# Kernel optimization log

Hardware: AMD Instinct MI355X
Metric: run time of the kernel (lower is better)

## Reference

```python
import jax, jax.numpy as jnp
import numpy as np

# --- model dims (from init_kwargs: d_model=2048, num_heads=16, d_conv=4, expand_v=2) ---
D_MODEL = 2048
N_HEADS = 16
D_HEAD = D_MODEL // N_HEADS          # 128
EXPAND_V = 2
KEY_DIM = N_HEADS * D_HEAD           # 2048
VALUE_DIM = KEY_DIM * EXPAND_V       # 4096
HEAD_V = D_HEAD * EXPAND_V           # 256
D_CONV = 4
CONV_CH = 2 * KEY_DIM + VALUE_DIM    # 8192 (q,k,v channels)
TOTAL_PROJ = 2 * KEY_DIM + 2 * VALUE_DIM + 2 * N_HEADS  # 12320
SPLITS = np.cumsum([KEY_DIM, KEY_DIM, VALUE_DIM, VALUE_DIM, N_HEADS]).tolist()


def setup_inputs() -> dict:
    key = jax.random.key(0)
    k0, k1, k2, k3 = jax.random.split(key, 4)
    B, L = 2, 2048
    return {
        "hidden_states": jax.random.normal(k0, (B, L, D_MODEL), jnp.float32),
        "W_qkvgba": jax.random.normal(k1, (D_MODEL, TOTAL_PROJ), jnp.float32) * 0.02,
        "W_conv": jax.random.normal(k2, (CONV_CH, D_CONV), jnp.float32) * 0.1,
        "A_log": jax.random.normal(k3, (N_HEADS,), jnp.float32) * 0.1,
        "dt_bias": jnp.zeros((N_HEADS,), jnp.float32),
    }


def _l2norm(x, eps=1e-6):
    return x * jax.lax.rsqrt(jnp.sum(x * x, axis=-1, keepdims=True) + eps)


def reference(hidden_states, W_qkvgba, W_conv, A_log, dt_bias):
    B, L, _ = hidden_states.shape
    # fused qkv / gate / beta / A projection
    proj = hidden_states @ W_qkvgba                      # [B, L, 12320]
    q, k, v, gate, b, A = jnp.split(proj, SPLITS, axis=-1)

    # depthwise causal short conv over q,k,v channels, then SiLU
    qkv = jnp.concatenate([q, k, v], axis=-1)            # [B, L, CONV_CH]
    x = qkv.transpose(0, 2, 1)                           # [B, C, L]
    kern = W_conv[:, None, :]                            # [C, 1, D_CONV]
    y = jax.lax.conv_general_dilated(
        x, kern, window_strides=(1,), padding=[(D_CONV - 1, 0)],
        feature_group_count=CONV_CH)
    y = jax.nn.silu(y).transpose(0, 2, 1)                # [B, L, C]
    q, k, v = jnp.split(y, [KEY_DIM, 2 * KEY_DIM], axis=-1)

    q = q.reshape(B, L, N_HEADS, D_HEAD)
    k = k.reshape(B, L, N_HEADS, D_HEAD)
    v = v.reshape(B, L, N_HEADS, HEAD_V)

    # L2 norm of q,k (use_qk_l2norm_in_kernel=True)
    q = _l2norm(q)
    k = _l2norm(k)
    scale = D_HEAD ** -0.5

    beta = jax.nn.sigmoid(b)                             # [B, L, H]
    g = -jnp.exp(A_log) * jax.nn.softplus(A + dt_bias)   # [B, L, H] (log decay <= 0)

    # gated delta-rule recurrence over time (scan); state S: [B, H, dk, dv]
    qT = q.transpose(1, 0, 2, 3)
    kT = k.transpose(1, 0, 2, 3)
    vT = v.transpose(1, 0, 2, 3)
    gT = g.transpose(1, 0, 2)
    bT = beta.transpose(1, 0, 2)

    def step(S, inp):
        qt, kt, vt, gt, bt = inp
        S = S * jnp.exp(gt)[..., None, None]
        kv = jnp.einsum('bhk,bhkv->bhv', kt, S)          # current memory readout at k
        delta = (vt - kv) * bt[..., None]                # delta-rule error, gated by beta
        S = S + jnp.einsum('bhk,bhv->bhkv', kt, delta)
        ot = jnp.einsum('bhk,bhkv->bhv', qt * scale, S)
        return S, ot

    S0 = jnp.zeros((B, N_HEADS, D_HEAD, HEAD_V), jnp.float32)
    _, oT = jax.lax.scan(step, S0, (qT, kT, vT, gT, bT))
    o = oT.transpose(1, 0, 2, 3)                         # [B, L, H, HEAD_V]

    # output gating: o * silu(gate)
    gate = gate.reshape(B, L, N_HEADS, HEAD_V)
    return o * jax.nn.silu(gate)
```

## Files before the change

### kernel.cpp

```cpp
#include <hip/hip_runtime.h>
#include <hip/hip_bf16.h>
#include <hip/hip_fp16.h>
#include <math.h>

#define L_SEQ 2048
#define DM    2048
#define NH    16
#define DH    128
#define HVD   256
#define NPROJ 12320
#define QKVW  8192
#define GW    4128

#define NTILE_N 97
#define KSTEPS  64

typedef _Float16 v8h __attribute__((ext_vector_type(8)));
typedef float f32x4 __attribute__((ext_vector_type(4)));

__device__ __forceinline__ void gload_lds16(const void* g, void* l) {
  __builtin_amdgcn_global_load_lds((const __attribute__((address_space(1))) void*)g,
                                   (__attribute__((address_space(3))) void*)l, 16, 0, 0);
}

__device__ __forceinline__ void splitw(float x, unsigned short& h, unsigned short& l) {
  _Float16 hh = (_Float16)x;
  _Float16 ll = (_Float16)(x - (float)hh);
  h = *(unsigned short*)&hh;
  l = *(unsigned short*)&ll;
}
__device__ __forceinline__ float h2f(unsigned short u) {
  return (float)(*(_Float16*)&u);
}

#define MFMA3(acc, ah, al, bh_, bl_)                                          \
  acc = __builtin_amdgcn_mfma_f32_16x16x32_f16(ah, bh_, acc, 0, 0, 0);        \
  acc = __builtin_amdgcn_mfma_f32_16x16x32_f16(ah, bl_, acc, 0, 0, 0);        \
  acc = __builtin_amdgcn_mfma_f32_16x16x32_f16(al, bh_, acc, 0, 0, 0);

__global__ __launch_bounds__(256) void pack_A_k(const float* __restrict__ H, _Float16* __restrict__ Ap) {
  const int mtile = blockIdx.x >> 6, kstep = blockIdx.x & 63;
  const size_t base = (size_t)blockIdx.x * 2 * 4096;
#pragma unroll
  for (int it = 0; it < 2; ++it) {
    int s = threadIdx.x + it * 256;
    int g = s >> 7, r = s & 127;
    const float* src = H + ((size_t)(mtile * 128 + r)) * 2048 + kstep * 32 + g * 8;
    float4 x0 = *(const float4*)src;
    float4 x1 = *(const float4*)(src + 4);
    float xs[8] = {x0.x, x0.y, x0.z, x0.w, x1.x, x1.y, x1.z, x1.w};
    v8h hi, lo;
#pragma unroll
    for (int j = 0; j < 8; ++j) {
      float v = xs[j] * 16.f;
      _Float16 h = (_Float16)v;
      hi[j] = h;
      lo[j] = (_Float16)(v - (float)h);
    }
    *(v8h*)(Ap + base + g * 1024 + r * 8) = hi;
    *(v8h*)(Ap + base + 4096 + g * 1024 + r * 8) = lo;
  }
}

__global__ __launch_bounds__(256) void pack_B_k(const float* __restrict__ W, _Float16* __restrict__ Bp) {
  const int ntile = blockIdx.x >> 6, kstep = blockIdx.x & 63;
  const size_t base = (size_t)blockIdx.x * 2 * 4096;
#pragma unroll
  for (int it = 0; it < 2; ++it) {
    int s = threadIdx.x + it * 256;
    int g = s >> 7, col = s & 127;
    int n = ntile * 128 + col;
    v8h hi, lo;
#pragma unroll
    for (int j = 0; j < 8; ++j) {
      int k = kstep * 32 + g * 8 + j;
      float v = (n < NPROJ) ? W[(size_t)k * NPROJ + n] * 1024.f : 0.f;
      _Float16 h = (_Float16)v;
      hi[j] = h;
      lo[j] = (_Float16)(v - (float)h);
    }
    *(v8h*)(Bp + base + g * 1024 + col * 8) = hi;
    *(v8h*)(Bp + base + 4096 + g * 1024 + col * 8) = lo;
  }
}

__global__ __launch_bounds__(512, 2) void gemm256_k(const _Float16* __restrict__ Ap,
                                                    const _Float16* __restrict__ Bp,
                                                    float* __restrict__ Cq,
                                                    float* __restrict__ Cg) {
  __shared__ _Float16 lds[2][32768];
  const int tid = threadIdx.x;
  const int supM = blockIdx.x & 15;
  const int supN = blockIdx.x >> 4;
  const int w = tid >> 6, lane = tid & 63;
  const int wm = w >> 2, wn = w & 3;
  const int lr = lane & 15, g16 = lane >> 4;

  f32x4 acc[8][4];
#pragma unroll
  for (int i = 0; i < 8; ++i)
#pragma unroll
    for (int j = 0; j < 4; ++j) acc[i][j] = (f32x4){0.f, 0.f, 0.f, 0.f};

  const size_t Ab0 = (size_t)(2 * supM) * KSTEPS * 8192;
  const size_t Ab1 = Ab0 + (size_t)KSTEPS * 8192;
  const size_t Bb0 = (size_t)(2 * supN) * KSTEPS * 8192;
  const size_t Bb1 = Bb0 + (size_t)KSTEPS * 8192;
  const int so = tid * 8;

#define STG(KS, BUF)                                                           \
  {                                                                            \
    const size_t ko = (size_t)(KS) * 8192;                                     \
    gload_lds16(Ap + Ab0 + ko + so,        &lds[BUF][so]);                     \
    gload_lds16(Ap + Ab0 + ko + so + 4096, &lds[BUF][so + 4096]);              \
    gload_lds16(Ap + Ab1 + ko + so,        &lds[BUF][8192 + so]);              \
    gload_lds16(Ap + Ab1 + ko + so + 4096, &lds[BUF][8192 + so + 4096]);       \
    gload_lds16(Bp + Bb0 + ko + so,        &lds[BUF][16384 + so]);             \
    gload_lds16(Bp + Bb0 + ko + so + 4096, &lds[BUF][16384 + so + 4096]);      \
    gload_lds16(Bp + Bb1 + ko + so,        &lds[BUF][24576 + so]);             \
    gload_lds16(Bp + Bb1 + ko + so + 4096, &lds[BUF][24576 + so + 4096]);      \
  }

  STG(0, 0);
  asm volatile("s_waitcnt vmcnt(0)" ::: "memory");
  __builtin_amdgcn_sched_barrier(0);
  __builtin_amdgcn_s_barrier();
  __builtin_amdgcn_sched_barrier(0);

  const int aoffB = wm * 8192 + lr * 8 + g16 * 1024;
  const int boffB = 16384 + (wn >> 1) * 8192 + ((wn & 1) * 64 + lr) * 8 + g16 * 1024;

  for (int kstep = 0; kstep < KSTEPS; ++kstep) {
    const int p = kstep & 1;
    if (kstep + 1 < KSTEPS) STG(kstep + 1, p ^ 1);

    v8h ah[8], al[8];
#pragma unroll
    for (int mb = 0; mb < 8; ++mb) {
      ah[mb] = *(const v8h*)&lds[p][aoffB + mb * 128];
      al[mb] = *(const v8h*)&lds[p][aoffB + mb * 128 + 4096];
    }
#pragma unroll
    for (int nt = 0; nt < 4; ++nt) {
      v8h bh = *(const v8h*)&lds[p][boffB + nt * 128];
      v8h bl = *(const v8h*)&lds[p][boffB + nt * 128 + 4096];
#pragma unroll
      for (int mb = 0; mb < 8; ++mb) {
        MFMA3(acc[mb][nt], ah[mb], al[mb], bh, bl);
      }
    }
    asm volatile("s_waitcnt vmcnt(0)" ::: "memory");
    __builtin_amdgcn_sched_barrier(0);
    __builtin_amdgcn_s_barrier();
    __builtin_amdgcn_sched_barrier(0);
  }
#undef STG

  const float sc = 1.f / 16384.f;
#pragma unroll
  for (int mb = 0; mb < 8; ++mb) {
#pragma unroll
    for (int nt = 0; nt < 4; ++nt) {
      int col = supN * 256 + wn * 64 + nt * 16 + lr;
#pragma unroll
      for (int r = 0; r < 4; ++r) {
        int row = supM * 256 + wm * 128 + mb * 16 + g16 * 4 + r;
        float v = acc[mb][nt][r] * sc;
        if (col < QKVW) Cq[(size_t)row * QKVW + col] = v;
        else            Cg[(size_t)row * GW + (col - QKVW)] = v;
      }
    }
  }
}

__global__ __launch_bounds__(256) void tail_k(const _Float16* __restrict__ Ap,
                                              const _Float16* __restrict__ Bp,
                                              float* __restrict__ partial) {
  __shared__ _Float16 lds[16384];
  const int bid = blockIdx.x;
  const int kseg = bid >> 5, mtile = bid & 31;
  const int tid = threadIdx.x;
  const int wid = tid >> 6, lane = tid & 63, lr = lane & 15, g16 = lane >> 4;

  f32x4 acc[2][2];
#pragma unroll
  for (int i = 0; i < 2; ++i)
#pragma unroll
    for (int j = 0; j < 2; ++j) acc[i][j] = (f32x4){0.f, 0.f, 0.f, 0.f};

  const _Float16* Asrc = Ap + ((size_t)(mtile * KSTEPS) * 2) * 4096 + tid * 8;
  const _Float16* Bsrc = Bp + ((size_t)(96 * KSTEPS) * 2) * 4096 + tid * 8;

  for (int ks = kseg * 16; ks < kseg * 16 + 16; ++ks) {
    __syncthreads();
#pragma unroll
    for (int r = 0; r < 4; ++r) {
      gload_lds16(Asrc + (size_t)ks * 8192 + r * 2048, &lds[r * 2048 + tid * 8]);
      gload_lds16(Bsrc + (size_t)ks * 8192 + r * 2048, &lds[8192 + r * 2048 + tid * 8]);
    }
    __syncthreads();
    const int abase = g16 * 1024;
#pragma unroll
    for (int fm = 0; fm < 2; ++fm) {
      int row = wid * 32 + fm * 16 + lr;
      v8h ah = *(const v8h*)&lds[abase + row * 8];
      v8h al = *(const v8h*)&lds[4096 + abase + row * 8];
#pragma unroll
      for (int fn = 0; fn < 2; ++fn) {
        int col = fn * 16 + lr;
        v8h bh = *(const v8h*)&lds[8192 + abase + col * 8];
        v8h bl = *(const v8h*)&lds[12288 + abase + col * 8];
        MFMA3(acc[fm][fn], ah, al, bh, bl);
      }
    }
  }

  const float sc = 1.f / 16384.f;
#pragma unroll
  for (int fm = 0; fm < 2; ++fm)
#pragma unroll
    for (int fn = 0; fn < 2; ++fn) {
      int col = fn * 16 + lr;
#pragma unroll
      for (int r = 0; r < 4; ++r) {
        int row = mtile * 128 + wid * 32 + fm * 16 + g16 * 4 + r;
        partial[((size_t)kseg * 4096 + row) * 32 + col] = acc[fm][fn][r] * sc;
      }
    }
}

__global__ __launch_bounds__(64) void conv_qk_k(
    const float* __restrict__ projQKV, const float* __restrict__ Wc,
    _Float16* __restrict__ qh, _Float16* __restrict__ ql,
    _Float16* __restrict__ kh, _Float16* __restrict__ kl)
{
  const int b = blockIdx.z, hg = blockIdx.y, tc = blockIdx.x;
  const int lane = threadIdx.x;
  const int ch = hg * 128 + lane * 2;
  float4 Wa = *(const float4*)(Wc + (size_t)ch * 4);
  float4 Wb = *(const float4*)(Wc + (size_t)ch * 4 + 4);
  const int t0 = tc * 64;
  const float* P = projQKV + (size_t)b * L_SEQ * QKVW + ch;
  float2 w0 = make_float2(0.f, 0.f), w1 = w0, w2 = w0;
  if (t0 >= 3) w0 = *(const float2*)(P + (size_t)(t0 - 3) * QKVW);
  if (t0 >= 2) w1 = *(const float2*)(P + (size_t)(t0 - 2) * QKVW);
  if (t0 >= 1) w2 = *(const float2*)(P + (size_t)(t0 - 1) * QKVW);
  const bool isq = hg < 16;
  const int h = isq ? hg : hg - 16;
  _Float16* dh = (isq ? qh : kh) + (((size_t)b * NH + h) * L_SEQ) * 128;
  _Float16* dl = (isq ? ql : kl) + (((size_t)b * NH + h) * L_SEQ) * 128;
  const float sc = (isq ? 0.08838834764831845f : 1.f) * 1024.f;
  for (int t = t0; t < t0 + 64; ++t) {
    float2 x = *(const float2*)(P + (size_t)t * QKVW);
    float y0 = w0.x * Wa.x + w1.x * Wa.y + w2.x * Wa.z + x.x * Wa.w;
    float y1 = w0.y * Wb.x + w1.y * Wb.y + w2.y * Wb.z + x.y * Wb.w;
    w0 = w1; w1 = w2; w2 = x;
    y0 = y0 / (1.f + expf(-y0));
    y1 = y1 / (1.f + expf(-y1));
    float ss = y0 * y0 + y1 * y1;
#pragma unroll
    for (int off = 1; off < 64; off <<= 1) ss += __shfl_xor(ss, off);
    float nrm = sc / sqrtf(ss + 1e-6f);
    unsigned short h0, l0, h1, l1;
    splitw(y0 * nrm, h0, l0);
    splitw(y1 * nrm, h1, l1);
    int idx = t * 128 + ((lane * 2) ^ ((t & 7) << 3));
    *(unsigned int*)&dh[idx] = (unsigned int)h0 | ((unsigned int)h1 << 16);
    *(unsigned int*)&dl[idx] = (unsigned int)l0 | ((unsigned int)l1 << 16);
  }
}

__global__ __launch_bounds__(256) void conv_v_k(
    const float* __restrict__ projQKV, const float* __restrict__ Wc,
    float* __restrict__ vn)
{
  const int b = blockIdx.z, cg = blockIdx.y, tc = blockIdx.x;
  const int vc = (cg * 256 + threadIdx.x) * 4;
  const int ch = 4096 + vc;
  float4 Wv0 = *(const float4*)(Wc + (size_t)ch * 4);
  float4 Wv1 = *(const float4*)(Wc + (size_t)ch * 4 + 4);
  float4 Wv2 = *(const float4*)(Wc + (size_t)ch * 4 + 8);
  float4 Wv3 = *(const float4*)(Wc + (size_t)ch * 4 + 12);
  const int t0 = tc * 64;
  const float* P = projQKV + (size_t)b * L_SEQ * QKVW + ch;
  float4 w0 = make_float4(0.f, 0.f, 0.f, 0.f), w1 = w0, w2 = w0;
  if (t0 >= 3) w0 = *(const float4*)(P + (size_t)(t0 - 3) * QKVW);
  if (t0 >= 2) w1 = *(const float4*)(P + (size_t)(t0 - 2) * QKVW);
  if (t0 >= 1) w2 = *(const float4*)(P + (size_t)(t0 - 1) * QKVW);
  const int h = vc >> 8, vcol = vc & 255;
  float* dst = vn + (((size_t)b * NH + h) * L_SEQ) * HVD + vcol;
  for (int t = t0; t < t0 + 64; ++t) {
    float4 x = *(const float4*)(P + (size_t)t * QKVW);
    float4 y;
    y.x = w0.x * Wv0.x + w1.x * Wv0.y + w2.x * Wv0.z + x.x * Wv0.w;
    y.y = w0.y * Wv1.x + w1.y * Wv1.y + w2.y * Wv1.z + x.y * Wv1.w;
    y.z = w0.z * Wv2.x + w1.z * Wv2.y + w2.z * Wv2.z + x.z * Wv2.w;
    y.w = w0.w * Wv3.x + w1.w * Wv3.y + w2.w * Wv3.z + x.w * Wv3.w;
    w0 = w1; w1 = w2; w2 = x;
    y.x = y.x / (1.f + expf(-y.x));
    y.y = y.y / (1.f + expf(-y.y));
    y.z = y.z / (1.f + expf(-y.z));
    y.w = y.w / (1.f + expf(-y.w));
    *(float4*)(dst + (size_t)t * HVD) = y;
  }
}

__global__ __launch_bounds__(256) void beta_g_k(
    const float* __restrict__ partial, const float* __restrict__ A_log,
    const float* __restrict__ dt_bias, float* __restrict__ beta, float* __restrict__ g_out)
{
  int idx = blockIdx.x * 256 + threadIdx.x;
  if (idx >= 2 * NH * L_SEQ) return;
  int t = idx & (L_SEQ - 1);
  int h = (idx >> 11) & (NH - 1);
  int b = idx >> 15;
  size_t row = (size_t)(b * L_SEQ + t);
  float bv = 0.f, av = 0.f;
#pragma unroll
  for (int s = 0; s < 4; ++s) {
    bv += partial[((size_t)s * 4096 + row) * 32 + h];
    av += partial[((size_t)s * 4096 + row) * 32 + 16 + h];
  }
  float be = 1.f / (1.f + expf(-bv));
  float xx = av + dt_bias[h];
  float sp = (xx > 20.f) ? xx : log1pf(expf(xx));
  float g = -expf(A_log[h]) * sp;
  beta[idx] = be;
  g_out[idx] = g;
}

__global__ __launch_bounds__(256) void p1_k(
    const _Float16* __restrict__ kh_g, const _Float16* __restrict__ kl_g,
    const _Float16* __restrict__ qh_g, const _Float16* __restrict__ ql_g,
    const float* __restrict__ g_arr, const float* __restrict__ beta_arr,
    _Float16* __restrict__ Tg_h, _Float16* __restrict__ Tg_l,
    _Float16* __restrict__ Hg_h, _Float16* __restrict__ Hg_l,
    _Float16* __restrict__ KTg_h, _Float16* __restrict__ KTg_l,
    float* __restrict__ coefG)
{
  __shared__ _Float16 Kh[8192], Kl[8192];
  __shared__ _Float16 QS[16384];
  __shared__ float lc[64], be[64], kw[64];
  _Float16* Qh = QS;
  _Float16* Ql = QS + 8192;
  float* Am = (float*)QS;
  float* Tm = Am + 4096;
  const int cid = blockIdx.x, bh = cid >> 5, ch = cid & 31, t0 = ch * 64;
  const int tid = threadIdx.x, w = tid >> 6, lane = tid & 63, lr = lane & 15, g16 = lane >> 4;

  const size_t gb = ((size_t)bh * 2048 + t0) * 128;
#pragma unroll
  for (int l = 0; l < 4; ++l) {
    int i = (tid + l * 256) * 8;
    gload_lds16(kh_g + gb + i, &Kh[i]);
    gload_lds16(kl_g + gb + i, &Kl[i]);
    gload_lds16(qh_g + gb + i, &Qh[i]);
    gload_lds16(ql_g + gb + i, &Ql[i]);
  }
  if (tid < 64) {
    float x = g_arr[(size_t)bh * 2048 + t0 + tid];
#pragma unroll
    for (int off = 1; off < 64; off <<= 1) { float y = __shfl_up(x, off); if (tid >= off) x += y; }
    lc[tid] = x;
    float x63 = __shfl(x, 63);
    float b_ = beta_arr[(size_t)bh * 2048 + t0 + tid];
    be[tid] = b_;
    kw[tid] = expf(x63 - x);
    float ca = expf(x);
    coefG[(size_t)cid * 192 + tid] = ca;
    coefG[(size_t)cid * 192 + 64 + tid] = b_;
    coefG[(size_t)cid * 192 + 128 + tid] = b_ * ca;
  }
  __syncthreads();
  const float ds20 = 1.f / 1048576.f;
  const int arow = w * 16 + lr, swa = (arow & 7) << 3;
  f32x4 gacc[4];
  for (int nt = 0; nt < 4; ++nt) {
    f32x4 acc = (f32x4){0.f, 0.f, 0.f, 0.f};
    int nrow = nt * 16 + lr, swn = (nrow & 7) << 3;
#pragma unroll
    for (int ks = 0; ks < 4; ++ks) {
      int c = ks * 32 + g16 * 8;
      v8h ah = *(const v8h*)&Kh[arow * 128 + (c ^ swa)];
      v8h al = *(const v8h*)&Kl[arow * 128 + (c ^ swa)];
      v8h bhh = *(const v8h*)&Kh[nrow * 128 + (c ^ swn)];
      v8h bll = *(const v8h*)&Kl[nrow * 128 + (c ^ swn)];
      MFMA3(acc, ah, al, bhh, bll);
    }
    gacc[nt] = acc;
  }
  for (int nt = 0; nt < 4; ++nt) {
    f32x4 acc = (f32x4){0.f, 0.f, 0.f, 0.f};
    int nrow = nt * 16 + lr, swn = (nrow & 7) << 3;
#pragma unroll
    for (int ks = 0; ks < 4; ++ks) {
      int c = ks * 32 + g16 * 8;
      v8h ah = *(const v8h*)&Qh[arow * 128 + (c ^ swa)];
      v8h al = *(const v8h*)&Ql[arow * 128 + (c ^ swa)];
      v8h bhh = *(const v8h*)&Kh[nrow * 128 + (c ^ swn)];
      v8h bll = *(const v8h*)&Kl[nrow * 128 + (c ^ swn)];
      MFMA3(acc, ah, al, bhh, bll);
    }
    int s_ = nt * 16 + lr;
#pragma unroll
    for (int r = 0; r < 4; ++r) {
      int t = w * 16 + g16 * 4 + r;
      float hv = (s_ <= t) ? acc[r] * ds20 * expf(lc[t] - lc[s_]) : 0.f;
      unsigned short hh, ll; splitw(hv * 16384.f, hh, ll);
      size_t go = (size_t)cid * 4096 + t * 64 + (s_ ^ ((t & 7) << 3));
      *(unsigned short*)&Hg_h[go] = hh;
      *(unsigned short*)&Hg_l[go] = ll;
    }
  }
  __syncthreads();
  for (int nt = 0; nt < 4; ++nt) {
    int s_ = nt * 16 + lr;
#pragma unroll
    for (int r = 0; r < 4; ++r) {
      int t = w * 16 + g16 * 4 + r;
      float av = (s_ < t) ? gacc[nt][r] * ds20 * be[t] * expf(lc[t] - lc[s_]) : 0.f;
      Am[t * 64 + s_] = av;
    }
  }
#pragma unroll
  for (int l = 0; l < 16; ++l) { int s2 = tid + l * 256; Tm[s2] = ((s2 >> 6) == (s2 & 63)) ? 1.f : 0.f; }
  for (int s = tid; s < 8192; s += 256) {
    int feat = s >> 6, t = s & 63;
    int ki = t * 128 + (feat ^ ((t & 7) << 3));
    float kvv = ((float)Kh[ki] + (float)Kl[ki]) * kw[t];
    unsigned short hh, ll; splitw(kvv, hh, ll);
    size_t go = (size_t)cid * 8192 + feat * 64 + (t ^ ((feat & 7) << 3));
    *(unsigned short*)&KTg_h[go] = hh;
    *(unsigned short*)&KTg_l[go] = ll;
  }
  __syncthreads();
  if (w == 0) {
    int j = lane;
    for (int t = 1; t < 64; ++t) {
      float sum = 0.f;
      for (int s = 0; s < t; ++s) sum = fmaf(Am[t * 64 + s], Tm[s * 64 + j], sum);
      Tm[t * 64 + j] = ((j == t) ? 1.f : 0.f) - sum;
    }
  }
  __syncthreads();
#pragma unroll
  for (int l = 0; l < 16; ++l) {
    int s2 = tid + l * 256;
    int t = s2 >> 6, sc_ = s2 & 63;
    unsigned short hh, ll; splitw(Tm[s2] * 256.f, hh, ll);
    size_t go = (size_t)cid * 4096 + t * 64 + (sc_ ^ ((t & 7) << 3));
    *(unsigned short*)&Tg_h[go] = hh;
    *(unsigned short*)&Tg_l[go] = ll;
  }
}

__global__ __launch_bounds__(256) void p2_k(
    const _Float16* __restrict__ qh_g, const _Float16* __restrict__ ql_g,
    const _Float16* __restrict__ kh_g, const _Float16* __restrict__ kl_g,
    const float* __restrict__ vn, const float* __restrict__ projGate,
    const _Float16* __restrict__ Tg_h, const _Float16* __restrict__ Tg_l,
    const _Float16* __restrict__ Hg_h, const _Float16* __restrict__ Hg_l,
    const _Float16* __restrict__ KTg_h, const _Float16* __restrict__ KTg_l,
    const float* __restrict__ coefG, float* __restrict__ out)
{
  __shared__ _Float16 St_h[4096], St_l[4096];
  __shared__ _Float16 KQ0[8192], KQ1[8192];
  __shared__ _Float16 KK0[8192], KK1[8192];
  __shared__ _Float16 KTs_h[8192], KTs_l[8192];
  __shared__ _Float16 Ts_h[4096], Ts_l[4096];
  __shared__ _Float16 Hs_h[4096], Hs_l[4096];
  __shared__ float cf[192];

  const int blk = blockIdx.x;
  const int vb = blk >> 5, bh = blk & 31;
  const int b = bh >> 4, h = bh & 15, v0 = vb * 32;
  const int tid = threadIdx.x, w = tid >> 6, lane = tid & 63, lr = lane & 15, g16 = lane >> 4;

  _Float16* BT_h = &KQ0[0];
  _Float16* BT_l = &KQ0[4096];
  _Float16* UT_h = &KQ1[0];
  _Float16* UT_l = &KQ1[4096];

#pragma unroll
  for (int l = 0; l < 8; ++l) { ((unsigned int*)St_h)[tid + l * 256] = 0u; }
#pragma unroll
  for (int l = 0; l < 8; ++l) { ((unsigned int*)St_l)[tid + l * 256] = 0u; }

  const float* gp = projGate + ((size_t)b * 2048) * GW + h * 256 + v0;
  const float i2_16 = 1.f / 65536.f;
  const float i2_20 = 1.f / 1048576.f;
  const float uscale = 1.f / 256.f;
  const float sscale = 64.f / 65536.f;

  for (int ch = 0; ch < 32; ++ch) {
    const int cid = bh * 32 + ch, t0 = ch * 64;
    {
      const _Float16* th = Tg_h + (size_t)cid * 4096;
      const _Float16* tl = Tg_l + (size_t)cid * 4096;
      const _Float16* hh = Hg_h + (size_t)cid * 4096;
      const _Float16* hl = Hg_l + (size_t)cid * 4096;
      const _Float16* kth = KTg_h + (size_t)cid * 8192;
      const _Float16* ktl = KTg_l + (size_t)cid * 8192;
      const size_t gb = ((size_t)bh * 2048 + t0) * 128;
#pragma unroll
      for (int l = 0; l < 2; ++l) {
        int i = (tid + l * 256) * 8;
        gload_lds16(th + i, &Ts_h[i]);
        gload_lds16(tl + i, &Ts_l[i]);
        gload_lds16(hh + i, &Hs_h[i]);
        gload_lds16(hl + i, &Hs_l[i]);
      }
#pragma unroll
      for (int l = 0; l < 4; ++l) {
        int i = (tid + l * 256) * 8;
        gload_lds16(kth + i, &KTs_h[i]);
        gload_lds16(ktl + i, &KTs_l[i]);
        gload_lds16(qh_g + gb + i, &KQ0[i]);
        gload_lds16(ql_g + gb + i, &KQ1[i]);
        gload_lds16(kh_g + gb + i, &KK0[i]);
        gload_lds16(kl_g + gb + i, &KK1[i]);
      }
      if (tid < 48) gload_lds16(coefG + (size_t)cid * 192 + tid * 4, &cf[tid * 4]);
    }
    float Vv[2][4];
#pragma unroll
    for (int nt = 0; nt < 2; ++nt)
#pragma unroll
      for (int r = 0; r < 4; ++r)
        Vv[nt][r] = vn[((size_t)bh * 2048 + t0 + w * 16 + g16 * 4 + r) * 256 + v0 + nt * 16 + lr];
    __syncthreads();
    const float cc = cf[63];
    const int arow = w * 16 + lr, swa = (arow & 7) << 3;
    f32x4 Oacc[2];
    {
      for (int nt = 0; nt < 2; ++nt) {
        f32x4 acc = (f32x4){0.f, 0.f, 0.f, 0.f};
        const int n = nt * 16 + lr, swn = (n & 7) << 3;
#pragma unroll
        for (int ks = 0; ks < 4; ++ks) {
          int c = ks * 32 + g16 * 8;
          v8h ah = *(const v8h*)&KQ0[arow * 128 + (c ^ swa)];
          v8h al = *(const v8h*)&KQ1[arow * 128 + (c ^ swa)];
          v8h bhh = *(const v8h*)&St_h[n * 128 + (c ^ swn)];
          v8h bll = *(const v8h*)&St_l[n * 128 + (c ^ swn)];
          MFMA3(acc, ah, al, bhh, bll);
        }
        Oacc[nt] = acc;
      }
      float4 cav = *(float4*)&cf[w * 16 + g16 * 4];
#pragma unroll
      for (int nt = 0; nt < 2; ++nt) {
        Oacc[nt][0] *= cav.x * 16.f; Oacc[nt][1] *= cav.y * 16.f;
        Oacc[nt][2] *= cav.z * 16.f; Oacc[nt][3] *= cav.w * 16.f;
      }
    }
    ushort4 pBh[2], pBl[2];
    {
      float4 cb1v = *(float4*)&cf[64 + w * 16 + g16 * 4];
      float4 cb2v = *(float4*)&cf[128 + w * 16 + g16 * 4];
      for (int nt = 0; nt < 2; ++nt) {
        f32x4 acc = (f32x4){0.f, 0.f, 0.f, 0.f};
        const int n = nt * 16 + lr, swn = (n & 7) << 3;
#pragma unroll
        for (int ks = 0; ks < 4; ++ks) {
          int c = ks * 32 + g16 * 8;
          v8h ah = *(const v8h*)&KK0[arow * 128 + (c ^ swa)];
          v8h al = *(const v8h*)&KK1[arow * 128 + (c ^ swa)];
          v8h bhh = *(const v8h*)&St_h[n * 128 + (c ^ swn)];
          v8h bll = *(const v8h*)&St_l[n * 128 + (c ^ swn)];
          MFMA3(acc, ah, al, bhh, bll);
        }
        float cb1a[4] = {cb1v.x, cb1v.y, cb1v.z, cb1v.w};
        float cb2a[4] = {cb2v.x, cb2v.y, cb2v.z, cb2v.w};
        unsigned short* ph = (unsigned short*)&pBh[nt];
        unsigned short* pl = (unsigned short*)&pBl[nt];
#pragma unroll
        for (int r = 0; r < 4; ++r) {
          float kv = acc[r] * i2_16;
          float Bv = cb1a[r] * Vv[nt][r] - cb2a[r] * kv;
          splitw(Bv * 64.f, ph[r], pl[r]);
        }
      }
    }
    __syncthreads();
    {
      const int tb = w * 16 + g16 * 4;
      for (int nt = 0; nt < 2; ++nt) {
        const int n = nt * 16 + lr, swn = (n & 7) << 3;
        int ad = n * 64 + (tb ^ swn);
        *(ushort4*)&BT_h[ad] = pBh[nt];
        *(ushort4*)&BT_l[ad] = pBl[nt];
      }
    }
    __syncthreads();
    {
      const int tb = w * 16 + g16 * 4;
      for (int nt = 0; nt < 2; ++nt) {
        f32x4 acc = (f32x4){0.f, 0.f, 0.f, 0.f};
        const int n = nt * 16 + lr, swn = (n & 7) << 3;
#pragma unroll
        for (int ks = 0; ks < 2; ++ks) {
          int c = ks * 32 + g16 * 8;
          v8h ah = *(const v8h*)&Ts_h[arow * 64 + (c ^ swa)];
          v8h al = *(const v8h*)&Ts_l[arow * 64 + (c ^ swa)];
          v8h bhh = *(const v8h*)&BT_h[n * 64 + (c ^ swn)];
          v8h bll = *(const v8h*)&BT_l[n * 64 + (c ^ swn)];
          MFMA3(acc, ah, al, bhh, bll);
        }
        ushort4 H, L;
        unsigned short* ph = (unsigned short*)&H;
        unsigned short* pl = (unsigned short*)&L;
#pragma unroll
        for (int r = 0; r < 4; ++r) splitw(acc[r] * uscale, ph[r], pl[r]);
        int ad = n * 64 + (tb ^ swn);
        *(ushort4*)&UT_h[ad] = H;
        *(ushort4*)&UT_l[ad] = L;
      }
    }
    __syncthreads();
    {
      for (int nt = 0; nt < 2; ++nt) {
        const int n = nt * 16 + lr, swn = (n & 7) << 3;
#pragma unroll
        for (int ks = 0; ks < 2; ++ks) {
          int c = ks * 32 + g16 * 8;
          v8h ah = *(const v8h*)&Hs_h[arow * 64 + (c ^ swa)];
          v8h al = *(const v8h*)&Hs_l[arow * 64 + (c ^ swa)];
          v8h bhh = *(const v8h*)&UT_h[n * 64 + (c ^ swn)];
          v8h bll = *(const v8h*)&UT_l[n * 64 + (c ^ swn)];
          MFMA3(Oacc[nt], ah, al, bhh, bll);
        }
      }
      for (int nt = 0; nt < 2; ++nt) {
        const int n = nt * 16 + lr;
#pragma unroll
        for (int r = 0; r < 4; ++r) {
          int t = t0 + w * 16 + g16 * 4 + r;
          float Ov = Oacc[nt][r] * i2_20;
          float gv = gp[(size_t)t * GW + n];
          out[((size_t)b * 2048 + t) * 4096 + h * 256 + v0 + n] = Ov * (gv / (1.f + expf(-gv)));
        }
      }
      const float cc1024 = cc * 1024.f;
#pragma unroll
      for (int m2 = w * 2; m2 < w * 2 + 2; ++m2) {
        const int ar2 = m2 * 16 + lr, swa2 = (ar2 & 7) << 3;
        const int fb = m2 * 16 + g16 * 4;
        for (int nt = 0; nt < 2; ++nt) {
          const int n = nt * 16 + lr, swn = (n & 7) << 3;
          int sad = n * 128 + (fb ^ swn);
          ushort4 sh4 = *(ushort4*)&St_h[sad];
          ushort4 sl4 = *(ushort4*)&St_l[sad];
          f32x4 acc;
          acc[0] = cc1024 * (h2f(sh4.x) + h2f(sl4.x));
          acc[1] = cc1024 * (h2f(sh4.y) + h2f(sl4.y));
          acc[2] = cc1024 * (h2f(sh4.z) + h2f(sl4.z));
          acc[3] = cc1024 * (h2f(sh4.w) + h2f(sl4.w));
#pragma unroll
          for (int ks = 0; ks < 2; ++ks) {
            int c = ks * 32 + g16 * 8;
            v8h ah = *(const v8h*)&KTs_h[ar2 * 64 + (c ^ swa2)];
            v8h al = *(const v8h*)&KTs_l[ar2 * 64 + (c ^ swa2)];
            v8h bhh = *(const v8h*)&UT_h[n * 64 + (c ^ swn)];
            v8h bll = *(const v8h*)&UT_l[n * 64 + (c ^ swn)];
            MFMA3(acc, ah, al, bhh, bll);
          }
          ushort4 H, L;
          unsigned short* ph = (unsigned short*)&H;
          unsigned short* pl = (unsigned short*)&L;
#pragma unroll
          for (int r = 0; r < 4; ++r) splitw(acc[r] * sscale, ph[r], pl[r]);
          *(ushort4*)&St_h[sad] = H;
          *(ushort4*)&St_l[sad] = L;
        }
      }
    }
    __syncthreads();
  }
}

extern "C" void kernel_launch(void* const* d_in, const int* in_sizes, int n_in,
                              void* d_out, int out_size, void* d_ws, size_t ws_size,
                              hipStream_t stream) {
  const float* hidden  = (const float*)d_in[0];
  const float* W       = (const float*)d_in[1];
  const float* Wc      = (const float*)d_in[2];
  const float* A_log   = (const float*)d_in[3];
  const float* dt_bias = (const float*)d_in[4];
  float* out = (float*)d_out;

  char* ws = (char*)d_ws;
  _Float16* Ap = (_Float16*)ws;
  _Float16* Bp = (_Float16*)(ws + (size_t)33554432);
  float* partial = (float*)(ws + (size_t)33554432);
  _Float16* qh = (_Float16*)ws;
  _Float16* ql = (_Float16*)(ws + (size_t)16777216);
  _Float16* kh = (_Float16*)(ws + (size_t)33554432);
  _Float16* kl = (_Float16*)(ws + (size_t)50331648);
  float* vn    = (float*)(ws + (size_t)67108864);
  float* g_arr = (float*)(ws + (size_t)134217728);
  float* beta  = (float*)(ws + (size_t)134479872);
  float* projQKV = (float*)(ws + (size_t)135266304);
  char*  tb0 = ws + (size_t)135266304;
  _Float16* Tg_h  = (_Float16*)tb0;
  _Float16* Tg_l  = (_Float16*)(tb0 + (size_t)8388608);
  _Float16* Hg_h  = (_Float16*)(tb0 + (size_t)16777216);
  _Float16* Hg_l  = (_Float16*)(tb0 + (size_t)25165824);
  _Float16* KTg_h = (_Float16*)(tb0 + (size_t)33554432);
  _Float16* KTg_l = (_Float16*)(tb0 + (size_t)50331648);
  float*    coefG = (float*)   (tb0 + (size_t)67108864);
  float* projGate = (float*)(ws + (size_t)269484032);

  pack_A_k<<<32 * KSTEPS, 256, 0, stream>>>(hidden, Ap);
  pack_B_k<<<NTILE_N * KSTEPS, 256, 0, stream>>>(W, Bp);
  gemm256_k<<<768, 512, 0, stream>>>(Ap, Bp, projQKV, projGate);
  tail_k<<<128, 256, 0, stream>>>(Ap, Bp, partial);
  beta_g_k<<<(2 * NH * L_SEQ + 255) / 256, 256, 0, stream>>>(partial, A_log, dt_bias, beta, g_arr);

  conv_qk_k<<<dim3(32, 32, 2), 64, 0, stream>>>(projQKV, Wc, qh, ql, kh, kl);
  conv_v_k<<<dim3(32, 4, 2), 256, 0, stream>>>(projQKV, Wc, vn);

  p1_k<<<1024, 256, 0, stream>>>(kh, kl, qh, ql, g_arr, beta, Tg_h, Tg_l, Hg_h, Hg_l, KTg_h, KTg_l, coefG);
  p2_k<<<256, 256, 0, stream>>>(qh, ql, kh, kl, vn, projGate, Tg_h, Tg_l, Hg_h, Hg_l, KTg_h, KTg_l, coefG, out);
}
```

Baseline: 927.9 us.

## Read chunk operands directly from global memory instead of staging in LDS

The chunked recurrence kernel no longer stages Q, K, T, H, KT tiles and coefficients into shared memory through async global-to-LDS loads. Each wave now reads its MFMA A-operands straight from global memory (mostly L2 hits), and BT and UT get their own small LDS buffers. This cuts LDS from about 150KB to 48KB so more blocks can share a CU, and it drops one barrier per chunk. The cost is that every wave issues its own global loads with the swizzle pattern baked in, exposing global latency on the serial chunk path with no prefetch.

```diff
diff --git a/kernel.cpp b/kernel.cpp
--- a/kernel.cpp
+++ b/kernel.cpp
@@ -464,73 +464,49 @@
     const float* __restrict__ coefG, float* __restrict__ out)
 {
   __shared__ _Float16 St_h[4096], St_l[4096];
-  __shared__ _Float16 KQ0[8192], KQ1[8192];
-  __shared__ _Float16 KK0[8192], KK1[8192];
-  __shared__ _Float16 KTs_h[8192], KTs_l[8192];
-  __shared__ _Float16 Ts_h[4096], Ts_l[4096];
-  __shared__ _Float16 Hs_h[4096], Hs_l[4096];
-  __shared__ float cf[192];
+  __shared__ _Float16 BT_h[4096], BT_l[4096];
+  __shared__ _Float16 UT_h[4096], UT_l[4096];
 
   const int blk = blockIdx.x;
   const int vb = blk >> 5, bh = blk & 31;
   const int b = bh >> 4, h = bh & 15, v0 = vb * 32;
   const int tid = threadIdx.x, w = tid >> 6, lane = tid & 63, lr = lane & 15, g16 = lane >> 4;
 
-  _Float16* BT_h = &KQ0[0];
-  _Float16* BT_l = &KQ0[4096];
-  _Float16* UT_h = &KQ1[0];
-  _Float16* UT_l = &KQ1[4096];
-
 #pragma unroll
   for (int l = 0; l < 8; ++l) { ((unsigned int*)St_h)[tid + l * 256] = 0u; }
 #pragma unroll
   for (int l = 0; l < 8; ++l) { ((unsigned int*)St_l)[tid + l * 256] = 0u; }
+  __syncthreads();
 
   const float* gp = projGate + ((size_t)b * 2048) * GW + h * 256 + v0;
   const float i2_16 = 1.f / 65536.f;
   const float i2_20 = 1.f / 1048576.f;
   const float uscale = 1.f / 256.f;
   const float sscale = 64.f / 65536.f;
+  const int arow = w * 16 + lr, swa = (arow & 7) << 3;
+  const int tb = w * 16 + g16 * 4;
 
   for (int ch = 0; ch < 32; ++ch) {
     const int cid = bh * 32 + ch, t0 = ch * 64;
-    {
-      const _Float16* th = Tg_h + (size_t)cid * 4096;
-      const _Float16* tl = Tg_l + (size_t)cid * 4096;
-      const _Float16* hh = Hg_h + (size_t)cid * 4096;
-      const _Float16* hl = Hg_l + (size_t)cid * 4096;
-      const _Float16* kth = KTg_h + (size_t)cid * 8192;
-      const _Float16* ktl = KTg_l + (size_t)cid * 8192;
-      const size_t gb = ((size_t)bh * 2048 + t0) * 128;
-#pragma unroll
-      for (int l = 0; l < 2; ++l) {
-        int i = (tid + l * 256) * 8;
-        gload_lds16(th + i, &Ts_h[i]);
-        gload_lds16(tl + i, &Ts_l[i]);
-        gload_lds16(hh + i, &Hs_h[i]);
-        gload_lds16(hl + i, &Hs_l[i]);
-      }
-#pragma unroll
-      for (int l = 0; l < 4; ++l) {
-        int i = (tid + l * 256) * 8;
-        gload_lds16(kth + i, &KTs_h[i]);
-        gload_lds16(ktl + i, &KTs_l[i]);
-        gload_lds16(qh_g + gb + i, &KQ0[i]);
-        gload_lds16(ql_g + gb + i, &KQ1[i]);
-        gload_lds16(kh_g + gb + i, &KK0[i]);
-        gload_lds16(kl_g + gb + i, &KK1[i]);
-      }
-      if (tid < 48) gload_lds16(coefG + (size_t)cid * 192 + tid * 4, &cf[tid * 4]);
-    }
+    const size_t gb = ((size_t)bh * 2048 + t0) * 128;
+    const _Float16* Tb = Tg_h + (size_t)cid * 4096;
+    const _Float16* Tbl = Tg_l + (size_t)cid * 4096;
+    const _Float16* Hb = Hg_h + (size_t)cid * 4096;
+    const _Float16* Hbl = Hg_l + (size_t)cid * 4096;
+    const _Float16* KTb = KTg_h + (size_t)cid * 8192;
+    const _Float16* KTbl = KTg_l + (size_t)cid * 8192;
+    const float* cfp = coefG + (size_t)cid * 192;
+    const float cc = cfp[63];
+    float4 cav = *(const float4*)&cfp[w * 16 + g16 * 4];
+    float4 cb1v = *(const float4*)&cfp[64 + w * 16 + g16 * 4];
+    float4 cb2v = *(const float4*)&cfp[128 + w * 16 + g16 * 4];
     float Vv[2][4];
 #pragma unroll
     for (int nt = 0; nt < 2; ++nt)
 #pragma unroll
       for (int r = 0; r < 4; ++r)
         Vv[nt][r] = vn[((size_t)bh * 2048 + t0 + w * 16 + g16 * 4 + r) * 256 + v0 + nt * 16 + lr];
-    __syncthreads();
-    const float cc = cf[63];
-    const int arow = w * 16 + lr, swa = (arow & 7) << 3;
+
     f32x4 Oacc[2];
     {
       for (int nt = 0; nt < 2; ++nt) {
@@ -539,15 +515,14 @@
 #pragma unroll
         for (int ks = 0; ks < 4; ++ks) {
           int c = ks * 32 + g16 * 8;
-          v8h ah = *(const v8h*)&KQ0[arow * 128 + (c ^ swa)];
-          v8h al = *(const v8h*)&KQ1[arow * 128 + (c ^ swa)];
+          v8h ah = *(const v8h*)(qh_g + gb + arow * 128 + (c ^ swa));
+          v8h al = *(const v8h*)(ql_g + gb + arow * 128 + (c ^ swa));
           v8h bhh = *(const v8h*)&St_h[n * 128 + (c ^ swn)];
           v8h bll = *(const v8h*)&St_l[n * 128 + (c ^ swn)];
           MFMA3(acc, ah, al, bhh, bll);
         }
         Oacc[nt] = acc;
       }
-      float4 cav = *(float4*)&cf[w * 16 + g16 * 4];
 #pragma unroll
       for (int nt = 0; nt < 2; ++nt) {
         Oacc[nt][0] *= cav.x * 16.f; Oacc[nt][1] *= cav.y * 16.f;
@@ -556,22 +531,20 @@
     }
     ushort4 pBh[2], pBl[2];
     {
-      float4 cb1v = *(float4*)&cf[64 + w * 16 + g16 * 4];
-      float4 cb2v = *(float4*)&cf[128 + w * 16 + g16 * 4];
+      float cb1a[4] = {cb1v.x, cb1v.y, cb1v.z, cb1v.w};
+      float cb2a[4] = {cb2v.x, cb2v.y, cb2v.z, cb2v.w};
       for (int nt = 0; nt < 2; ++nt) {
         f32x4 acc = (f32x4){0.f, 0.f, 0.f, 0.f};
         const int n = nt * 16 + lr, swn = (n & 7) << 3;
 #pragma unroll
         for (int ks = 0; ks < 4; ++ks) {
           int c = ks * 32 + g16 * 8;
-          v8h ah = *(const v8h*)&KK0[arow * 128 + (c ^ swa)];
-          v8h al = *(const v8h*)&KK1[arow * 128 + (c ^ swa)];
+          v8h ah = *(const v8h*)(kh_g + gb + arow * 128 + (c ^ swa));
+          v8h al = *(const v8h*)(kl_g + gb + arow * 128 + (c ^ swa));
           v8h bhh = *(const v8h*)&St_h[n * 128 + (c ^ swn)];
           v8h bll = *(const v8h*)&St_l[n * 128 + (c ^ swn)];
           MFMA3(acc, ah, al, bhh, bll);
         }
-        float cb1a[4] = {cb1v.x, cb1v.y, cb1v.z, cb1v.w};
-        float cb2a[4] = {cb2v.x, cb2v.y, cb2v.z, cb2v.w};
         unsigned short* ph = (unsigned short*)&pBh[nt];
         unsigned short* pl = (unsigned short*)&pBl[nt];
 #pragma unroll
@@ -581,10 +554,6 @@
           splitw(Bv * 64.f, ph[r], pl[r]);
         }
       }
-    }
-    __syncthreads();
-    {
-      const int tb = w * 16 + g16 * 4;
       for (int nt = 0; nt < 2; ++nt) {
         const int n = nt * 16 + lr, swn = (n & 7) << 3;
         int ad = n * 64 + (tb ^ swn);
@@ -594,15 +563,14 @@
     }
     __syncthreads();
     {
-      const int tb = w * 16 + g16 * 4;
       for (int nt = 0; nt < 2; ++nt) {
         f32x4 acc = (f32x4){0.f, 0.f, 0.f, 0.f};
         const int n = nt * 16 + lr, swn = (n & 7) << 3;
 #pragma unroll
         for (int ks = 0; ks < 2; ++ks) {
           int c = ks * 32 + g16 * 8;
-          v8h ah = *(const v8h*)&Ts_h[arow * 64 + (c ^ swa)];
-          v8h al = *(const v8h*)&Ts_l[arow * 64 + (c ^ swa)];
+          v8h ah = *(const v8h*)(Tb + arow * 64 + (c ^ swa));
+          v8h al = *(const v8h*)(Tbl + arow * 64 + (c ^ swa));
           v8h bhh = *(const v8h*)&BT_h[n * 64 + (c ^ swn)];
           v8h bll = *(const v8h*)&BT_l[n * 64 + (c ^ swn)];
           MFMA3(acc, ah, al, bhh, bll);
@@ -624,8 +592,8 @@
 #pragma unroll
         for (int ks = 0; ks < 2; ++ks) {
           int c = ks * 32 + g16 * 8;
-          v8h ah = *(const v8h*)&Hs_h[arow * 64 + (c ^ swa)];
-          v8h al = *(const v8h*)&Hs_l[arow * 64 + (c ^ swa)];
+          v8h ah = *(const v8h*)(Hb + arow * 64 + (c ^ swa));
+          v8h al = *(const v8h*)(Hbl + arow * 64 + (c ^ swa));
           v8h bhh = *(const v8h*)&UT_h[n * 64 + (c ^ swn)];
           v8h bll = *(const v8h*)&UT_l[n * 64 + (c ^ swn)];
           MFMA3(Oacc[nt], ah, al, bhh, bll);
@@ -659,8 +627,8 @@
 #pragma unroll
           for (int ks = 0; ks < 2; ++ks) {
             int c = ks * 32 + g16 * 8;
-            v8h ah = *(const v8h*)&KTs_h[ar2 * 64 + (c ^ swa2)];
-            v8h al = *(const v8h*)&KTs_l[ar2 * 64 + (c ^ swa2)];
+            v8h ah = *(const v8h*)(KTb + ar2 * 64 + (c ^ swa2));
+            v8h al = *(const v8h*)(KTbl + ar2 * 64 + (c ^ swa2));
             v8h bhh = *(const v8h*)&UT_h[n * 64 + (c ^ swn)];
             v8h bll = *(const v8h*)&UT_l[n * 64 + (c ^ swn)];
             MFMA3(acc, ah, al, bhh, bll);
```

Result: slower. 1.015 ms (+9.3%).
